# Kernel optimization log

Measured on AMD Instinct MI355X. Metric: run time of the kernel, lower is better.

Reference implementation:

```python
import jax, jax.numpy as jnp
import numpy as np

NUM_NODES = 100000
NUM_EDGES = 600000
NUM_GRAPHS = 1000
EMB = 128


def setup_inputs() -> dict:
    key = jax.random.key(0)
    ks = jax.random.split(key, 12)
    x = jax.random.normal(ks[0], (NUM_NODES, 4), dtype=jnp.float32)
    edge_index = jax.random.randint(ks[1], (2, NUM_EDGES), 0, NUM_NODES, dtype=jnp.int32)
    x_scalar = jax.random.normal(ks[2], (NUM_GRAPHS, 4), dtype=jnp.float32)
    batch_index = jnp.sort(jax.random.randint(ks[3], (NUM_NODES,), 0, NUM_GRAPHS, dtype=jnp.int32))
    def glorot(k, shape):
        fan_in, fan_out = shape[0], shape[1]
        s = jnp.sqrt(2.0 / (fan_in + fan_out)).astype(jnp.float32)
        return jax.random.normal(k, shape, dtype=jnp.float32) * s
    return {
        "x": x,
        "edge_index": edge_index,
        "x_scalar": x_scalar,
        "batch_index": batch_index,
        "W0": glorot(ks[4], (4, EMB)), "b0": jnp.zeros((EMB,), jnp.float32),
        "W1": glorot(ks[5], (EMB, EMB)), "b1": jnp.zeros((EMB,), jnp.float32),
        "W2": glorot(ks[6], (EMB, EMB)), "b2": jnp.zeros((EMB,), jnp.float32),
        "W3": glorot(ks[7], (EMB, EMB)), "b3": jnp.zeros((EMB,), jnp.float32),
        "Wl1": glorot(ks[8], (EMB + 4, 64)), "bl1": jnp.zeros((64,), jnp.float32),
        "Wl2": glorot(ks[9], (64, 1)), "bl2": jnp.zeros((1,), jnp.float32),
    }


def _gcn_norm(edge_index, num_nodes):
    # PyG GCNConv default: add self-loops, symmetric normalization
    loop = jnp.arange(num_nodes, dtype=edge_index.dtype)
    src = jnp.concatenate([edge_index[0], loop])
    dst = jnp.concatenate([edge_index[1], loop])
    deg = jax.ops.segment_sum(jnp.ones_like(src, dtype=jnp.float32), dst,
                              num_segments=num_nodes)
    dinv = jnp.where(deg > 0, jax.lax.rsqrt(jnp.maximum(deg, 1e-12)), 0.0)
    norm = dinv[src] * dinv[dst]  # [E+N]
    return src, dst, norm


def _gcn_conv(h, src, dst, norm, W, b, num_nodes):
    h = h @ W                                   # [N, out]
    msg = h[src] * norm[:, None]                # gather + normalize
    out = jax.ops.segment_sum(msg, dst, num_segments=num_nodes)  # scatter-add
    return out + b


def reference(x, edge_index, x_scalar, batch_index,
              W0, b0, W1, b1, W2, b2, W3, b3, Wl1, bl1, Wl2, bl2):
    n = x.shape[0]
    src, dst, norm = _gcn_norm(edge_index, n)
    h = jax.nn.relu(_gcn_conv(x, src, dst, norm, W0, b0, n))
    h = jax.nn.relu(_gcn_conv(h, src, dst, norm, W1, b1, n))
    h = jax.nn.relu(_gcn_conv(h, src, dst, norm, W2, b2, n))
    h = jax.nn.relu(_gcn_conv(h, src, dst, norm, W3, b3, n))
    # global mean pool over batch_index
    sums = jax.ops.segment_sum(h, batch_index, num_segments=NUM_GRAPHS)
    cnts = jax.ops.segment_sum(jnp.ones((n,), jnp.float32), batch_index,
                               num_segments=NUM_GRAPHS)
    pooled = sums / jnp.maximum(cnts, 1.0)[:, None]          # [G, EMB]
    feat = jnp.concatenate([pooled, x_scalar], axis=1)       # [G, EMB+4]
    out = jax.nn.relu(feat @ Wl1 + bl1) @ Wl2 + bl2          # [G, 1]
    return out
```

## Files before the change

### kernel.cpp

```cpp
#include <hip/hip_runtime.h>

#define NN 100000
#define EE 600000
#define GG 1000
#define NB ((NN + 255) / 256)

typedef __bf16 bf16x8 __attribute__((ext_vector_type(8)));
typedef float f32x4 __attribute__((ext_vector_type(4)));
typedef unsigned int u32;

__device__ inline float2 bf2_to_f2(u32 u) {
  return make_float2(__uint_as_float(u << 16), __uint_as_float(u & 0xffff0000u));
}
__device__ inline u32 f2_to_bf2(float a, float b) {
  union { __bf16 h[2]; u32 u; } pk;
  pk.h[0] = (__bf16)a; pk.h[1] = (__bf16)b;
  return pk.u;
}


__global__ void k_init(int* cnt, int* fillc, int* gstart) {
  int i = blockIdx.x * 256 + threadIdx.x;
  if (i < NN) { cnt[i] = 0; fillc[i] = 0; }
  if (i <= GG) gstart[i] = NN;
}

__global__ void k_count(const int* __restrict__ dst, int* cnt) {
  int e = blockIdx.x * 256 + threadIdx.x;
  if (e < EE) atomicAdd(&cnt[dst[e]], 1);
}

__global__ void k_dinv(const int* __restrict__ cnt, float* dinv) {
  int i = blockIdx.x * 256 + threadIdx.x;
  if (i < NN) dinv[i] = rsqrtf((float)(cnt[i] + 1));
}

__global__ void k_scan1(const int* __restrict__ cnt, int* rowptr, int* bsum) {
  __shared__ int s[256];
  int tid = threadIdx.x;
  int i = blockIdx.x * 256 + tid;
  int v = (i < NN) ? cnt[i] : 0;
  s[tid] = v;
  __syncthreads();
  for (int off = 1; off < 256; off <<= 1) {
    int t = (tid >= off) ? s[tid - off] : 0;
    __syncthreads();
    s[tid] += t;
    __syncthreads();
  }
  if (i < NN) rowptr[i] = s[tid] - v;
  if (tid == 255) bsum[blockIdx.x] = s[255];
}

__global__ void k_scan2(int* bsum) {
  __shared__ int s[512];
  int tid = threadIdx.x;
  int v = (tid < NB) ? bsum[tid] : 0;
  s[tid] = v;
  __syncthreads();
  for (int off = 1; off < 512; off <<= 1) {
    int t = (tid >= off) ? s[tid - off] : 0;
    __syncthreads();
    s[tid] += t;
    __syncthreads();
  }
  if (tid < NB) bsum[tid] = s[tid] - v;
}

__global__ void k_scan3(int* rowptr, const int* __restrict__ bsum) {
  int i = blockIdx.x * 256 + threadIdx.x;
  if (i < NN) rowptr[i] += bsum[blockIdx.x];
  if (i == 0) rowptr[NN] = EE;
}

__global__ void k_fill(const int* __restrict__ src, const int* __restrict__ dst,
                       const int* __restrict__ rowptr, int* fillc,
                       const float* __restrict__ dinv,
                       int* csr_src, float* csr_w) {
  int e = blockIdx.x * 256 + threadIdx.x;
  if (e >= EE) return;
  int s = src[e], d = dst[e];
  int pos = rowptr[d] + atomicAdd(&fillc[d], 1);
  csr_src[pos] = s;
  csr_w[pos] = dinv[s] * dinv[d];
}

__global__ void k_gbound(const int* __restrict__ batch, int* gstart) {
  int i = blockIdx.x * 256 + threadIdx.x;
  if (i >= NN) return;
  int b = batch[i];
  if (i == 0) {
    for (int g = 0; g <= b; ++g) gstart[g] = 0;
  } else {
    int prev = batch[i - 1];
    for (int g = prev + 1; g <= b; ++g) gstart[g] = i;
  }
}

__global__ void k_wprep(const float* __restrict__ W, __bf16* __restrict__ Wt) {
  int idx = blockIdx.x * 256 + threadIdx.x;
  int n = idx >> 7, k = idx & 127;
  Wt[(size_t)n * 128 + k] = (__bf16)W[(size_t)k * 128 + n];
}


__global__ void k_mm0(const float* __restrict__ x, const float* __restrict__ W0,
                      __bf16* __restrict__ hout) {
  int idx = blockIdx.x * 256 + threadIdx.x;
  if (idx >= NN * 128) return;
  int node = idx >> 7, j = idx & 127;
  const float* xr = x + node * 4;
  float s = xr[0] * W0[j];
  s = fmaf(xr[1], W0[128 + j], s);
  s = fmaf(xr[2], W0[256 + j], s);
  s = fmaf(xr[3], W0[384 + j], s);
  hout[idx] = (__bf16)s;
}

#define LDSPAD 136
__global__ __launch_bounds__(256) void k_mfma(const __bf16* __restrict__ hin,
                                              const __bf16* __restrict__ Wt,
                                              __bf16* __restrict__ hout) {
  __shared__ __bf16 As[128 * LDSPAD];
  int tid = threadIdx.x;
  int row0 = blockIdx.x * 128;
  int lane = tid & 63, w = tid >> 6;
  int ln = lane & 15, quad = lane >> 4;

  bf16x8 bfrag[8][4];
  #pragma unroll
  for (int nt = 0; nt < 8; ++nt)
    #pragma unroll
    for (int kc = 0; kc < 4; ++kc)
      bfrag[nt][kc] = *(const bf16x8*)(Wt + (size_t)(nt * 16 + ln) * 128 + kc * 32 + quad * 8);

  #pragma unroll
  for (int i = 0; i < 8; ++i) {
    int eb = (i * 256 + tid) * 8;
    int r = eb >> 7, c = eb & 127;
    int gr = row0 + r;
    uint4 v = make_uint4(0, 0, 0, 0);
    if (gr < NN) v = *(const uint4*)(hin + (size_t)gr * 128 + c);
    *(uint4*)&As[r * LDSPAD + c] = v;
  }
  __syncthreads();

  f32x4 acc[2][8];
  #pragma unroll
  for (int rt = 0; rt < 2; ++rt)
    #pragma unroll
    for (int nt = 0; nt < 8; ++nt) acc[rt][nt] = (f32x4){0.f, 0.f, 0.f, 0.f};

  #pragma unroll
  for (int kc = 0; kc < 4; ++kc) {
    bf16x8 a0 = *(const bf16x8*)&As[(w * 32 + ln) * LDSPAD + kc * 32 + quad * 8];
    bf16x8 a1 = *(const bf16x8*)&As[(w * 32 + 16 + ln) * LDSPAD + kc * 32 + quad * 8];
    #pragma unroll
    for (int nt = 0; nt < 8; ++nt) {
      acc[0][nt] = __builtin_amdgcn_mfma_f32_16x16x32_bf16(a0, bfrag[nt][kc], acc[0][nt], 0, 0, 0);
      acc[1][nt] = __builtin_amdgcn_mfma_f32_16x16x32_bf16(a1, bfrag[nt][kc], acc[1][nt], 0, 0, 0);
    }
  }

  #pragma unroll
  for (int rt = 0; rt < 2; ++rt)
    #pragma unroll
    for (int nt = 0; nt < 8; ++nt)
      #pragma unroll
      for (int reg = 0; reg < 4; ++reg) {
        int gr = row0 + w * 32 + rt * 16 + quad * 4 + reg;
        if (gr < NN)
          hout[(size_t)gr * 128 + nt * 16 + ln] = (__bf16)acc[rt][nt][reg];
      }
}

__global__ __launch_bounds__(256) void k_aggregate(const u32* __restrict__ hlin2,
                                                   const int* __restrict__ rowptr,
                                                   const int* __restrict__ csr_src,
                                                   const float* __restrict__ csr_w,
                                                   const float* __restrict__ dinv,
                                                   const float* __restrict__ bias,
                                                   u32* __restrict__ hout2) {
  int node = blockIdx.x * 4 + (threadIdx.x >> 6);
  int lane = threadIdx.x & 63;
  if (node >= NN) return;
  float di = dinv[node];
  float sw = di * di;
  float2 hv = bf2_to_f2(hlin2[(size_t)node * 64 + lane]);
  float2 bv = *(const float2*)(bias + lane * 2);
  float2 acc = make_float2(fmaf(sw, hv.x, bv.x), fmaf(sw, hv.y, bv.y));
  int beg = rowptr[node], end = rowptr[node + 1];
  for (int base = beg; base < end; base += 64) {
    int m = end - base; if (m > 64) m = 64;
    int li = base + (lane < m ? lane : m - 1);
    int idxv = csr_src[li];
    int wbits = __float_as_int(csr_w[li]);
    int j = 0;
    for (; j + 4 <= m; j += 4) {
      int s0 = __builtin_amdgcn_readlane(idxv, j + 0);
      int s1 = __builtin_amdgcn_readlane(idxv, j + 1);
      int s2 = __builtin_amdgcn_readlane(idxv, j + 2);
      int s3 = __builtin_amdgcn_readlane(idxv, j + 3);
      float w0 = __int_as_float(__builtin_amdgcn_readlane(wbits, j + 0));
      float w1 = __int_as_float(__builtin_amdgcn_readlane(wbits, j + 1));
      float w2 = __int_as_float(__builtin_amdgcn_readlane(wbits, j + 2));
      float w3 = __int_as_float(__builtin_amdgcn_readlane(wbits, j + 3));
      u32 u0 = hlin2[(size_t)s0 * 64 + lane];
      u32 u1 = hlin2[(size_t)s1 * 64 + lane];
      u32 u2 = hlin2[(size_t)s2 * 64 + lane];
      u32 u3 = hlin2[(size_t)s3 * 64 + lane];
      float2 v0 = bf2_to_f2(u0), v1 = bf2_to_f2(u1);
      float2 v2 = bf2_to_f2(u2), v3 = bf2_to_f2(u3);
      acc.x = fmaf(w0, v0.x, acc.x); acc.y = fmaf(w0, v0.y, acc.y);
      acc.x = fmaf(w1, v1.x, acc.x); acc.y = fmaf(w1, v1.y, acc.y);
      acc.x = fmaf(w2, v2.x, acc.x); acc.y = fmaf(w2, v2.y, acc.y);
      acc.x = fmaf(w3, v3.x, acc.x); acc.y = fmaf(w3, v3.y, acc.y);
    }
    if (j + 2 <= m) {
      int s0 = __builtin_amdgcn_readlane(idxv, j + 0);
      int s1 = __builtin_amdgcn_readlane(idxv, j + 1);
      float w0 = __int_as_float(__builtin_amdgcn_readlane(wbits, j + 0));
      float w1 = __int_as_float(__builtin_amdgcn_readlane(wbits, j + 1));
      float2 v0 = bf2_to_f2(hlin2[(size_t)s0 * 64 + lane]);
      float2 v1 = bf2_to_f2(hlin2[(size_t)s1 * 64 + lane]);
      acc.x = fmaf(w0, v0.x, acc.x); acc.y = fmaf(w0, v0.y, acc.y);
      acc.x = fmaf(w1, v1.x, acc.x); acc.y = fmaf(w1, v1.y, acc.y);
      j += 2;
    }
    if (j < m) {
      int s0 = __builtin_amdgcn_readlane(idxv, j);
      float w0 = __int_as_float(__builtin_amdgcn_readlane(wbits, j));
      float2 v0 = bf2_to_f2(hlin2[(size_t)s0 * 64 + lane]);
      acc.x = fmaf(w0, v0.x, acc.x); acc.y = fmaf(w0, v0.y, acc.y);
    }
  }
  hout2[(size_t)node * 64 + lane] = f2_to_bf2(fmaxf(acc.x, 0.f), fmaxf(acc.y, 0.f));
}

__global__ __launch_bounds__(256) void k_poolmlp(const uint2* __restrict__ h4u,
                                                 const int* __restrict__ gstart,
                                                 const float* __restrict__ xs,
                                                 const float* __restrict__ Wl1,
                                                 const float* __restrict__ bl1,
                                                 const float* __restrict__ Wl2,
                                                 const float* __restrict__ bl2,
                                                 float* __restrict__ out) {
  __shared__ float4 part[8][32];
  __shared__ float pooled[128];
  int g = blockIdx.x;
  int beg = gstart[g], end = gstart[g + 1];
  int tid = threadIdx.x;
  int cg = tid & 31;
  int rg = tid >> 5;
  float4 acc = make_float4(0.f, 0.f, 0.f, 0.f);
  for (int i = beg + rg; i < end; i += 8) {
    uint2 u = h4u[(size_t)i * 32 + cg];
    acc.x += __uint_as_float(u.x << 16);
    acc.y += __uint_as_float(u.x & 0xffff0000u);
    acc.z += __uint_as_float(u.y << 16);
    acc.w += __uint_as_float(u.y & 0xffff0000u);
  }
  part[rg][cg] = acc;
  __syncthreads();
  if (tid < 32) {
    float4 s = part[0][tid];
    #pragma unroll
    for (int r = 1; r < 8; ++r) {
      float4 v = part[r][tid];
      s.x += v.x; s.y += v.y; s.z += v.z; s.w += v.w;
    }
    float sc = 1.f / fmaxf((float)(end - beg), 1.f);
    pooled[tid * 4 + 0] = s.x * sc;
    pooled[tid * 4 + 1] = s.y * sc;
    pooled[tid * 4 + 2] = s.z * sc;
    pooled[tid * 4 + 3] = s.w * sc;
  }
  __syncthreads();
  if (tid < 64) {
    float hj = bl1[tid];
    #pragma unroll 4
    for (int k = 0; k < 128; ++k) hj = fmaf(pooled[k], Wl1[k * 64 + tid], hj);
    const float* xr = xs + g * 4;
    #pragma unroll
    for (int k = 0; k < 4; ++k) hj = fmaf(xr[k], Wl1[(128 + k) * 64 + tid], hj);
    hj = fmaxf(hj, 0.f);
    float val = hj * Wl2[tid];
    #pragma unroll
    for (int off = 32; off > 0; off >>= 1) val += __shfl_down(val, off);
    if (tid == 0) out[g] = val + bl2[0];
  }
}


extern "C" void kernel_launch(void* const* d_in, const int* in_sizes, int n_in,
                              void* d_out, int out_size, void* d_ws, size_t ws_size,
                              hipStream_t stream) {
  const float* x    = (const float*)d_in[0];
  const int*   ei   = (const int*)d_in[1];
  const float* xs   = (const float*)d_in[2];
  const int*   batch= (const int*)d_in[3];
  const float* W0   = (const float*)d_in[4];
  const float* b0   = (const float*)d_in[5];
  const float* W1   = (const float*)d_in[6];
  const float* b1   = (const float*)d_in[7];
  const float* W2   = (const float*)d_in[8];
  const float* b2   = (const float*)d_in[9];
  const float* W3   = (const float*)d_in[10];
  const float* b3   = (const float*)d_in[11];
  const float* Wl1  = (const float*)d_in[12];
  const float* bl1  = (const float*)d_in[13];
  const float* Wl2  = (const float*)d_in[14];
  const float* bl2  = (const float*)d_in[15];
  const int* srcA = ei;
  const int* dstA = ei + EE;
  float* out = (float*)d_out;

  char* p = (char*)d_ws;
  auto take = [&](size_t bytes) { char* q = p; p += (bytes + 255) & ~(size_t)255; return q; };
  __bf16* hA   = (__bf16*)take((size_t)NN * 128 * 2);
  __bf16* hB   = (__bf16*)take((size_t)NN * 128 * 2);
  int*   cnt   = (int*)take((size_t)NN * 4);
  float* dinv  = (float*)take((size_t)NN * 4);
  int*   rowptr= (int*)take((size_t)(NN + 1) * 4);
  int*   fillc = (int*)take((size_t)NN * 4);
  int*   csr_s = (int*)take((size_t)EE * 4);
  float* csr_w = (float*)take((size_t)EE * 4);
  int*   bsum  = (int*)take(512 * 4);
  int*   gstart= (int*)take((size_t)(GG + 1) * 4);
  __bf16* Wt1  = (__bf16*)take(16384 * 2);
  __bf16* Wt2  = (__bf16*)take(16384 * 2);
  __bf16* Wt3  = (__bf16*)take(16384 * 2);

  k_init<<<NB, 256, 0, stream>>>(cnt, fillc, gstart);
  k_count<<<(EE + 255) / 256, 256, 0, stream>>>(dstA, cnt);
  k_dinv<<<NB, 256, 0, stream>>>(cnt, dinv);
  k_scan1<<<NB, 256, 0, stream>>>(cnt, rowptr, bsum);
  k_scan2<<<1, 512, 0, stream>>>(bsum);
  k_scan3<<<NB, 256, 0, stream>>>(rowptr, bsum);
  k_fill<<<(EE + 255) / 256, 256, 0, stream>>>(srcA, dstA, rowptr, fillc, dinv, csr_s, csr_w);
  k_gbound<<<NB, 256, 0, stream>>>(batch, gstart);
  k_wprep<<<64, 256, 0, stream>>>(W1, Wt1);
  k_wprep<<<64, 256, 0, stream>>>(W2, Wt2);
  k_wprep<<<64, 256, 0, stream>>>(W3, Wt3);

  k_mm0<<<(NN * 128 + 255) / 256, 256, 0, stream>>>(x, W0, hA);
  k_aggregate<<<(NN + 3) / 4, 256, 0, stream>>>((const u32*)hA, rowptr, csr_s, csr_w, dinv, b0, (u32*)hB);
  k_mfma<<<(NN + 127) / 128, 256, 0, stream>>>(hB, Wt1, hA);
  k_aggregate<<<(NN + 3) / 4, 256, 0, stream>>>((const u32*)hA, rowptr, csr_s, csr_w, dinv, b1, (u32*)hB);
  k_mfma<<<(NN + 127) / 128, 256, 0, stream>>>(hB, Wt2, hA);
  k_aggregate<<<(NN + 3) / 4, 256, 0, stream>>>((const u32*)hA, rowptr, csr_s, csr_w, dinv, b2, (u32*)hB);
  k_mfma<<<(NN + 127) / 128, 256, 0, stream>>>(hB, Wt3, hA);
  k_aggregate<<<(NN + 3) / 4, 256, 0, stream>>>((const u32*)hA, rowptr, csr_s, csr_w, dinv, b3, (u32*)hB);

  k_poolmlp<<<GG, 256, 0, stream>>>((const uint2*)hB, gstart, xs, Wl1, bl1, Wl2, bl2, out);
}
```

Before: 414.1 us.

## Pad CSR rows to multiples of eight and gather neighbours with 16-byte quad-split loads

The aggregation kernel now has each quarter-wavefront handle a different edge, loading whole 16-byte chunks of a neighbour row, and reduces the partial sums across quads with shuffles at the end. To make this branch-free, every CSR row is padded to a multiple of eight with zero-weight self entries. Source index and weight are packed into one int2 array. The degree-inverse computation is also folded into the first scan kernel. The aim is fewer, wider gather loads and less scalar readlane and tail-handling overhead. The cost is extra padded entries and a cross-lane reduction.

```diff
diff --git a/kernel.cpp b/kernel.cpp
--- a/kernel.cpp
+++ b/kernel.cpp
@@ -30,16 +30,13 @@
   if (e < EE) atomicAdd(&cnt[dst[e]], 1);
 }
 
-__global__ void k_dinv(const int* __restrict__ cnt, float* dinv) {
-  int i = blockIdx.x * 256 + threadIdx.x;
-  if (i < NN) dinv[i] = rsqrtf((float)(cnt[i] + 1));
-}
-
-__global__ void k_scan1(const int* __restrict__ cnt, int* rowptr, int* bsum) {
+__global__ void k_scan1(const int* __restrict__ cnt, float* __restrict__ dinv,
+                        int* rowptr, int* bsum) {
   __shared__ int s[256];
   int tid = threadIdx.x;
   int i = blockIdx.x * 256 + tid;
-  int v = (i < NN) ? cnt[i] : 0;
+  int v = (i < NN) ? ((cnt[i] + 7) & ~7) : 0;
+  if (i < NN) dinv[i] = rsqrtf((float)(cnt[i] + 1));
   s[tid] = v;
   __syncthreads();
   for (int off = 1; off < 256; off <<= 1) {
@@ -48,7 +45,7 @@
     s[tid] += t;
     __syncthreads();
   }
-  if (i < NN) rowptr[i] = s[tid] - v;
+  if (i <= NN) rowptr[i] = s[tid] - v;
   if (tid == 255) bsum[blockIdx.x] = s[255];
 }
 
@@ -69,20 +66,25 @@
 
 __global__ void k_scan3(int* rowptr, const int* __restrict__ bsum) {
   int i = blockIdx.x * 256 + threadIdx.x;
-  if (i < NN) rowptr[i] += bsum[blockIdx.x];
-  if (i == 0) rowptr[NN] = EE;
-}
-
-__global__ void k_fill(const int* __restrict__ src, const int* __restrict__ dst,
-                       const int* __restrict__ rowptr, int* fillc,
-                       const float* __restrict__ dinv,
-                       int* csr_src, float* csr_w) {
-  int e = blockIdx.x * 256 + threadIdx.x;
-  if (e >= EE) return;
-  int s = src[e], d = dst[e];
-  int pos = rowptr[d] + atomicAdd(&fillc[d], 1);
-  csr_src[pos] = s;
-  csr_w[pos] = dinv[s] * dinv[d];
+  if (i <= NN) rowptr[i] += bsum[blockIdx.x];
+}
+
+__global__ void k_fillpad(const int* __restrict__ src, const int* __restrict__ dst,
+                          const int* __restrict__ rowptr, int* fillc,
+                          const int* __restrict__ cnt,
+                          const float* __restrict__ dinv,
+                          int2* __restrict__ csr) {
+  int gid = blockIdx.x * 256 + threadIdx.x;
+  if (gid < EE) {
+    int s = src[gid], d = dst[gid];
+    int pos = rowptr[d] + atomicAdd(&fillc[d], 1);
+    csr[pos] = make_int2(s, __float_as_int(dinv[s] * dinv[d]));
+  }
+  if (gid < NN) {
+    int2 pad = make_int2(gid, 0);
+    for (int pos = rowptr[gid] + cnt[gid]; pos < rowptr[gid + 1]; ++pos)
+      csr[pos] = pad;
+  }
 }
 
 __global__ void k_gbound(const int* __restrict__ batch, int* gstart) {
@@ -174,67 +176,70 @@
       }
 }
 
-__global__ __launch_bounds__(256) void k_aggregate(const u32* __restrict__ hlin2,
+__global__ __launch_bounds__(256) void k_aggregate(const __bf16* __restrict__ hlin,
                                                    const int* __restrict__ rowptr,
-                                                   const int* __restrict__ csr_src,
-                                                   const float* __restrict__ csr_w,
+                                                   const int2* __restrict__ csr,
                                                    const float* __restrict__ dinv,
                                                    const float* __restrict__ bias,
                                                    u32* __restrict__ hout2) {
   int node = blockIdx.x * 4 + (threadIdx.x >> 6);
   int lane = threadIdx.x & 63;
+  int ln = lane & 15, quad = lane >> 4;
   if (node >= NN) return;
   float di = dinv[node];
   float sw = di * di;
-  float2 hv = bf2_to_f2(hlin2[(size_t)node * 64 + lane]);
-  float2 bv = *(const float2*)(bias + lane * 2);
-  float2 acc = make_float2(fmaf(sw, hv.x, bv.x), fmaf(sw, hv.y, bv.y));
+
+  uint4 su = *(const uint4*)(hlin + ((size_t)node << 7) + ln * 8);
+  float4 ba = *(const float4*)(bias + ln * 8);
+  float4 bb = *(const float4*)(bias + ln * 8 + 4);
+  float2 s0 = bf2_to_f2(su.x), s1 = bf2_to_f2(su.y);
+  float2 s2 = bf2_to_f2(su.z), s3 = bf2_to_f2(su.w);
+  float q0 = (quad == 0) ? 1.f : 0.f;
+  float acc[8];
+  acc[0] = q0 * fmaf(sw, s0.x, ba.x); acc[1] = q0 * fmaf(sw, s0.y, ba.y);
+  acc[2] = q0 * fmaf(sw, s1.x, ba.z); acc[3] = q0 * fmaf(sw, s1.y, ba.w);
+  acc[4] = q0 * fmaf(sw, s2.x, bb.x); acc[5] = q0 * fmaf(sw, s2.y, bb.y);
+  acc[6] = q0 * fmaf(sw, s3.x, bb.z); acc[7] = q0 * fmaf(sw, s3.y, bb.w);
+
   int beg = rowptr[node], end = rowptr[node + 1];
   for (int base = beg; base < end; base += 64) {
     int m = end - base; if (m > 64) m = 64;
     int li = base + (lane < m ? lane : m - 1);
-    int idxv = csr_src[li];
-    int wbits = __float_as_int(csr_w[li]);
-    int j = 0;
-    for (; j + 4 <= m; j += 4) {
-      int s0 = __builtin_amdgcn_readlane(idxv, j + 0);
-      int s1 = __builtin_amdgcn_readlane(idxv, j + 1);
-      int s2 = __builtin_amdgcn_readlane(idxv, j + 2);
-      int s3 = __builtin_amdgcn_readlane(idxv, j + 3);
-      float w0 = __int_as_float(__builtin_amdgcn_readlane(wbits, j + 0));
-      float w1 = __int_as_float(__builtin_amdgcn_readlane(wbits, j + 1));
-      float w2 = __int_as_float(__builtin_amdgcn_readlane(wbits, j + 2));
-      float w3 = __int_as_float(__builtin_amdgcn_readlane(wbits, j + 3));
-      u32 u0 = hlin2[(size_t)s0 * 64 + lane];
-      u32 u1 = hlin2[(size_t)s1 * 64 + lane];
-      u32 u2 = hlin2[(size_t)s2 * 64 + lane];
-      u32 u3 = hlin2[(size_t)s3 * 64 + lane];
-      float2 v0 = bf2_to_f2(u0), v1 = bf2_to_f2(u1);
-      float2 v2 = bf2_to_f2(u2), v3 = bf2_to_f2(u3);
-      acc.x = fmaf(w0, v0.x, acc.x); acc.y = fmaf(w0, v0.y, acc.y);
-      acc.x = fmaf(w1, v1.x, acc.x); acc.y = fmaf(w1, v1.y, acc.y);
-      acc.x = fmaf(w2, v2.x, acc.x); acc.y = fmaf(w2, v2.y, acc.y);
-      acc.x = fmaf(w3, v3.x, acc.x); acc.y = fmaf(w3, v3.y, acc.y);
+    int2 md = csr[li];
+    int idxv = md.x, wbits = md.y;
+    for (int j = 0; j < m; j += 8) {
+      int sl0 = (j + quad) * 4, sl1 = (j + 4 + quad) * 4;
+      int r0 = __builtin_amdgcn_ds_bpermute(sl0, idxv);
+      int r1 = __builtin_amdgcn_ds_bpermute(sl1, idxv);
+      float w0 = __int_as_float(__builtin_amdgcn_ds_bpermute(sl0, wbits));
+      float w1 = __int_as_float(__builtin_amdgcn_ds_bpermute(sl1, wbits));
+      uint4 u0 = *(const uint4*)(hlin + ((size_t)r0 << 7) + ln * 8);
+      uint4 u1 = *(const uint4*)(hlin + ((size_t)r1 << 7) + ln * 8);
+      float2 f;
+      f = bf2_to_f2(u0.x); acc[0] = fmaf(w0, f.x, acc[0]); acc[1] = fmaf(w0, f.y, acc[1]);
+      f = bf2_to_f2(u0.y); acc[2] = fmaf(w0, f.x, acc[2]); acc[3] = fmaf(w0, f.y, acc[3]);
+      f = bf2_to_f2(u0.z); acc[4] = fmaf(w0, f.x, acc[4]); acc[5] = fmaf(w0, f.y, acc[5]);
+      f = bf2_to_f2(u0.w); acc[6] = fmaf(w0, f.x, acc[6]); acc[7] = fmaf(w0, f.y, acc[7]);
+      f = bf2_to_f2(u1.x); acc[0] = fmaf(w1, f.x, acc[0]); acc[1] = fmaf(w1, f.y, acc[1]);
+      f = bf2_to_f2(u1.y); acc[2] = fmaf(w1, f.x, acc[2]); acc[3] = fmaf(w1, f.y, acc[3]);
+      f = bf2_to_f2(u1.z); acc[4] = fmaf(w1, f.x, acc[4]); acc[5] = fmaf(w1, f.y, acc[5]);
+      f = bf2_to_f2(u1.w); acc[6] = fmaf(w1, f.x, acc[6]); acc[7] = fmaf(w1, f.y, acc[7]);
     }
-    if (j + 2 <= m) {
-      int s0 = __builtin_amdgcn_readlane(idxv, j + 0);
-      int s1 = __builtin_amdgcn_readlane(idxv, j + 1);
-      float w0 = __int_as_float(__builtin_amdgcn_readlane(wbits, j + 0));
-      float w1 = __int_as_float(__builtin_amdgcn_readlane(wbits, j + 1));
-      float2 v0 = bf2_to_f2(hlin2[(size_t)s0 * 64 + lane]);
-      float2 v1 = bf2_to_f2(hlin2[(size_t)s1 * 64 + lane]);
-      acc.x = fmaf(w0, v0.x, acc.x); acc.y = fmaf(w0, v0.y, acc.y);
-      acc.x = fmaf(w1, v1.x, acc.x); acc.y = fmaf(w1, v1.y, acc.y);
-      j += 2;
-    }
-    if (j < m) {
-      int s0 = __builtin_amdgcn_readlane(idxv, j);
-      float w0 = __int_as_float(__builtin_amdgcn_readlane(wbits, j));
-      float2 v0 = bf2_to_f2(hlin2[(size_t)s0 * 64 + lane]);
-      acc.x = fmaf(w0, v0.x, acc.x); acc.y = fmaf(w0, v0.y, acc.y);
-    }
-  }
-  hout2[(size_t)node * 64 + lane] = f2_to_bf2(fmaxf(acc.x, 0.f), fmaxf(acc.y, 0.f));
+  }
+
+  #pragma unroll
+  for (int k = 0; k < 8; ++k) {
+    acc[k] += __shfl_xor(acc[k], 16);
+    acc[k] += __shfl_xor(acc[k], 32);
+  }
+  if (quad == 0) {
+    uint4 o;
+    o.x = f2_to_bf2(fmaxf(acc[0], 0.f), fmaxf(acc[1], 0.f));
+    o.y = f2_to_bf2(fmaxf(acc[2], 0.f), fmaxf(acc[3], 0.f));
+    o.z = f2_to_bf2(fmaxf(acc[4], 0.f), fmaxf(acc[5], 0.f));
+    o.w = f2_to_bf2(fmaxf(acc[6], 0.f), fmaxf(acc[7], 0.f));
+    *(uint4*)(hout2 + (size_t)node * 64 + ln * 4) = o;
+  }
 }
 
 __global__ __launch_bounds__(256) void k_poolmlp(const uint2* __restrict__ h4u,
@@ -323,8 +328,7 @@
   float* dinv  = (float*)take((size_t)NN * 4);
   int*   rowptr= (int*)take((size_t)(NN + 1) * 4);
   int*   fillc = (int*)take((size_t)NN * 4);
-  int*   csr_s = (int*)take((size_t)EE * 4);
-  float* csr_w = (float*)take((size_t)EE * 4);
+  int2*  csr   = (int2*)take((size_t)(EE + 7 * NN + 64) * 8);
   int*   bsum  = (int*)take(512 * 4);
   int*   gstart= (int*)take((size_t)(GG + 1) * 4);
   __bf16* Wt1  = (__bf16*)take(16384 * 2);
@@ -333,24 +337,23 @@
 
   k_init<<<NB, 256, 0, stream>>>(cnt, fillc, gstart);
   k_count<<<(EE + 255) / 256, 256, 0, stream>>>(dstA, cnt);
-  k_dinv<<<NB, 256, 0, stream>>>(cnt, dinv);
-  k_scan1<<<NB, 256, 0, stream>>>(cnt, rowptr, bsum);
+  k_scan1<<<NB, 256, 0, stream>>>(cnt, dinv, rowptr, bsum);
   k_scan2<<<1, 512, 0, stream>>>(bsum);
   k_scan3<<<NB, 256, 0, stream>>>(rowptr, bsum);
-  k_fill<<<(EE + 255) / 256, 256, 0, stream>>>(srcA, dstA, rowptr, fillc, dinv, csr_s, csr_w);
+  k_fillpad<<<(EE + 255) / 256, 256, 0, stream>>>(srcA, dstA, rowptr, fillc, cnt, dinv, csr);
   k_gbound<<<NB, 256, 0, stream>>>(batch, gstart);
   k_wprep<<<64, 256, 0, stream>>>(W1, Wt1);
   k_wprep<<<64, 256, 0, stream>>>(W2, Wt2);
   k_wprep<<<64, 256, 0, stream>>>(W3, Wt3);
 
   k_mm0<<<(NN * 128 + 255) / 256, 256, 0, stream>>>(x, W0, hA);
-  k_aggregate<<<(NN + 3) / 4, 256, 0, stream>>>((const u32*)hA, rowptr, csr_s, csr_w, dinv, b0, (u32*)hB);
+  k_aggregate<<<(NN + 3) / 4, 256, 0, stream>>>(hA, rowptr, csr, dinv, b0, (u32*)hB);
   k_mfma<<<(NN + 127) / 128, 256, 0, stream>>>(hB, Wt1, hA);
-  k_aggregate<<<(NN + 3) / 4, 256, 0, stream>>>((const u32*)hA, rowptr, csr_s, csr_w, dinv, b1, (u32*)hB);
+  k_aggregate<<<(NN + 3) / 4, 256, 0, stream>>>(hA, rowptr, csr, dinv, b1, (u32*)hB);
   k_mfma<<<(NN + 127) / 128, 256, 0, stream>>>(hB, Wt2, hA);
-  k_aggregate<<<(NN + 3) / 4, 256, 0, stream>>>((const u32*)hA, rowptr, csr_s, csr_w, dinv, b2, (u32*)hB);
+  k_aggregate<<<(NN + 3) / 4, 256, 0, stream>>>(hA, rowptr, csr, dinv, b2, (u32*)hB);
   k_mfma<<<(NN + 127) / 128, 256, 0, stream>>>(hB, Wt3, hA);
-  k_aggregate<<<(NN + 3) / 4, 256, 0, stream>>>((const u32*)hA, rowptr, csr_s, csr_w, dinv, b3, (u32*)hB);
+  k_aggregate<<<(NN + 3) / 4, 256, 0, stream>>>(hA, rowptr, csr, dinv, b3, (u32*)hB);
 
   k_poolmlp<<<GG, 256, 0, stream>>>((const uint2*)hB, gstart, xs, Wl1, bl1, Wl2, bl2, out);
 }
```

Measured after the change: 414.2 us. No clear change (+0.0%).
